# Kernel tuning notes

Hardware: AMD Instinct MI355X
Metric: run time of the kernel (lower is better)

## Reference

```python
import jax, jax.numpy as jnp
import numpy as np

B, N, F, I = 4, 1024, 32, 8
DIM, DN, NF = 256, 64, 100
H, HD = 4, 64  # heads, head_dim (H*HD == DIM)
EPS = 1e-5


def setup_inputs() -> dict:
    key = jax.random.key(0)
    ks = jax.random.split(key, 24)
    def p(k, shape, s=0.05):
        return jax.random.normal(k, shape, jnp.float32) * s
    return {
        "x": jax.random.normal(ks[0], (B, N, F, I), jnp.float32),
        "idx": jax.random.randint(ks[1], (F,), 0, NF),
        "ctx": jax.random.normal(ks[2], (B, 1, DN), jnp.float32),
        "Wp": p(ks[3], (NF, DIM * I)),          # in_projection table
        "Bp": p(ks[4], (NF, DIM)),               # feature_bias table
        "q_emb": p(ks[5], (1, DIM)),             # queries table
        "cln_kv_W": p(ks[6], (DN, 2 * DIM)), "cln_kv_b": jnp.zeros((2 * DIM,), jnp.float32),
        "cln_q_W": p(ks[7], (DN, 2 * DIM)),  "cln_q_b": jnp.zeros((2 * DIM,), jnp.float32),
        "cln_h_W": p(ks[8], (DN, 2 * DIM)),  "cln_h_b": jnp.zeros((2 * DIM,), jnp.float32),
        "Wq": p(ks[9], (DIM, DIM)), "Wk": p(ks[10], (DIM, DIM)),
        "Wv": p(ks[11], (DIM, DIM)), "Wo": p(ks[12], (DIM, DIM)),
        "W1": p(ks[13], (DIM, 4 * DIM)), "b1": jnp.zeros((4 * DIM,), jnp.float32),
        "W2": p(ks[14], (4 * DIM, DIM)), "b2": jnp.zeros((DIM,), jnp.float32),
    }


def _ln(x):
    m = x.mean(-1, keepdims=True)
    v = ((x - m) ** 2).mean(-1, keepdims=True)
    return (x - m) * jax.lax.rsqrt(v + EPS)


def _cln(x, c, W, b):
    # adaptive layernorm: ln(x) * (1 + scale(ctx)) + shift(ctx)
    h = _ln(x)
    s, sh = jnp.split(c @ W + b, 2, axis=-1)
    return h * (1.0 + s) + sh


def reference(x, idx, ctx, Wp, Bp, q_emb, cln_kv_W, cln_kv_b, cln_q_W, cln_q_b,
              cln_h_W, cln_h_b, Wq, Wk, Wv, Wo, W1, b1, W2, b2):
    b_, n_, f_, i_ = x.shape
    # gather per-feature projection weights and biases
    w = Wp[idx].reshape(f_, DIM, i_)                 # [f, d, i]
    bias = Bp[idx][None]                              # [1, f, d] (broadcasts b,n)
    kv = jnp.einsum('bnfi,fdi->bnfd', x, w)           # [b, n, f, d]
    c = ctx[:, :, None, :]                            # [b, 1, 1, dn]
    kv = _cln(kv, c, cln_kv_W, cln_kv_b) + bias
    q = jnp.broadcast_to(q_emb[None, None], (b_, n_, 1, DIM))
    # cross-attention (pre-norm, conditional)
    qn = _cln(q, c, cln_q_W, cln_q_b)
    qh = (qn @ Wq).reshape(b_, n_, 1, H, HD)
    kh = (kv @ Wk).reshape(b_, n_, f_, H, HD)
    vh = (kv @ Wv).reshape(b_, n_, f_, H, HD)
    att = jnp.einsum('bnqhe,bnfhe->bnhqf', qh, kh) / np.sqrt(HD).astype(np.float32)
    att = jax.nn.softmax(att, axis=-1)
    o = jnp.einsum('bnhqf,bnfhe->bnqhe', att, vh).reshape(b_, n_, 1, DIM) @ Wo
    h = q + o
    # MLP (pre-norm, conditional)
    hn = _cln(h, c, cln_h_W, cln_h_b)
    h = h + (jax.nn.gelu(hn @ W1 + b1) @ W2 + b2)
    return h[:, :, 0, :]                              # squeeze query dim -> [b, n, d]
```

## Files before the change

### kernel.cpp

```cpp
#include <hip/hip_runtime.h>
#include <cmath>

#define EPSV 1e-5f
using f4 = float4;

typedef __attribute__((ext_vector_type(8))) short bfrag;
typedef __attribute__((ext_vector_type(4))) float ffrag;

#define WS_SKV   0
#define WS_SHKV  1024
#define WS_SH    2048
#define WS_SHH   3072
#define WS_A     4096
#define WS_R     8192
#define WS_HT    4202496
#define WS_L     5251072
#define WS_G     6299648
#define WS_GB    WS_G
#define WS_HNB   (WS_G + 2097152)
#define WS_W1T   (WS_G + 2621440)
#define WS_W2T   (WS_G + 2752512)
#define WS_MT    (WS_G + 2883584)

#define FMA8(acc, s, wa, wb) \
  acc[0]=fmaf((s),(wa).x,acc[0]); acc[1]=fmaf((s),(wa).y,acc[1]); \
  acc[2]=fmaf((s),(wa).z,acc[2]); acc[3]=fmaf((s),(wa).w,acc[3]); \
  acc[4]=fmaf((s),(wb).x,acc[4]); acc[5]=fmaf((s),(wb).y,acc[5]); \
  acc[6]=fmaf((s),(wb).z,acc[6]); acc[7]=fmaf((s),(wb).w,acc[7]);

#define DOT8(res, v, wa, wb) \
  res = fmaf((v)[0],(wa).x,res); res = fmaf((v)[1],(wa).y,res); \
  res = fmaf((v)[2],(wa).z,res); res = fmaf((v)[3],(wa).w,res); \
  res = fmaf((v)[4],(wb).x,res); res = fmaf((v)[5],(wb).y,res); \
  res = fmaf((v)[6],(wb).z,res); res = fmaf((v)[7],(wb).w,res);

__device__ __forceinline__ float bfly32(float v){
  v += __shfl_xor(v, 1);  v += __shfl_xor(v, 2);  v += __shfl_xor(v, 4);
  v += __shfl_xor(v, 8);  v += __shfl_xor(v, 16);
  return v;
}

template<int CTRL>
__device__ __forceinline__ float dpp_add(float v){
  int x = __builtin_bit_cast(int, v);
  int y = __builtin_amdgcn_update_dpp(0, x, CTRL, 0xf, 0xf, true);
  return v + __builtin_bit_cast(float, y);
}
__device__ __forceinline__ float red32(float v){
  v = dpp_add<0xB1>(v);
  v = dpp_add<0x4E>(v);
  v = dpp_add<0x124>(v);
  v = dpp_add<0x128>(v);
  v += __shfl_xor(v, 16);
  return v;
}

__device__ __forceinline__ float gelu_fast(float x){
  float z2 = 1.5957691216057308f*(x + 0.044715f*x*x*x);
  return x / (1.0f + __expf(-z2));
}

__device__ __forceinline__ unsigned short f2bf(float x){
  union { float f; unsigned u; } v; v.f = x;
  unsigned r = v.u + 0x7fffu + ((v.u >> 16) & 1u);
  return (unsigned short)(r >> 16);
}
__device__ __forceinline__ float bfu(unsigned short u){
  union { unsigned u; float f; } v; v.u = ((unsigned)u) << 16; return v.f;
}
__device__ __forceinline__ ushort4 comb4(ushort4 a, ushort4 b, float inv){
  ushort4 r;
  r.x = f2bf((bfu(a.x)+bfu(b.x))*inv);
  r.y = f2bf((bfu(a.y)+bfu(b.y))*inv);
  r.z = f2bf((bfu(a.z)+bfu(b.z))*inv);
  r.w = f2bf((bfu(a.w)+bfu(b.w))*inv);
  return r;
}

__global__ __launch_bounds__(256) void kprep(
  const float* __restrict__ W1, const float* __restrict__ W2,
  const float* __restrict__ Wv, const float* __restrict__ Wo,
  const float* __restrict__ ctx, const float* __restrict__ q_emb,
  const float* __restrict__ Wkv, const float* __restrict__ bkv,
  const float* __restrict__ Wqc, const float* __restrict__ bqc,
  const float* __restrict__ Whc, const float* __restrict__ bhc,
  const float* __restrict__ Wq,  const float* __restrict__ Wk,
  float* __restrict__ ws)
{
  const int tid = threadIdx.x;
  int blk = blockIdx.x;
  __shared__ union {
    unsigned short lt[64][68];
    struct { float wvs[4*64]; float wos[64*256]; } m;
    struct { float c[64], qn[256], ph[256], qh64[64], red[8]; } z;
  } sm;

  if (blk < 128){
    const float* src; unsigned short* dst; int K, N, K0, N0;
    if (blk < 64){
      src = W1; dst = (unsigned short*)(ws + WS_W1T);
      K = 256; N = 1024; K0 = (blk >> 4)*64; N0 = (blk & 15)*64;
    } else {
      blk -= 64;
      src = W2; dst = (unsigned short*)(ws + WS_W2T);
      K = 1024; N = 256; K0 = (blk >> 2)*64; N0 = (blk & 3)*64;
    }
    #pragma unroll
    for (int i=0;i<4;++i){
      int r = i*16 + (tid>>4);
      int c = (tid&15)*4;
      f4 v = *(const f4*)(src + (size_t)(K0+r)*N + N0 + c);
      sm.lt[r][c]   = f2bf(v.x); sm.lt[r][c+1] = f2bf(v.y);
      sm.lt[r][c+2] = f2bf(v.z); sm.lt[r][c+3] = f2bf(v.w);
    }
    __syncthreads();
    #pragma unroll
    for (int i=0;i<4;++i){
      int n  = i*16 + (tid>>4);
      int kc = (tid&15)*4;
      ushort4 u;
      u.x = sm.lt[kc][n]; u.y = sm.lt[kc+1][n]; u.z = sm.lt[kc+2][n]; u.w = sm.lt[kc+3][n];
      *(ushort4*)(dst + (size_t)(N0+n)*K + K0 + kc) = u;
    }
  } else if (blk < 384){
    blk -= 128;
    const int h   = blk >> 6;
    const int dg4 = blk & 63;
    {
      int d = tid >> 6, e = tid & 63;
      sm.m.wvs[d*64+e] = Wv[(size_t)(dg4*4 + d)*256 + h*64 + e];
    }
    {
      int e = tid >> 2, c = (tid & 3)*64;
      const float* src = Wo + (size_t)(h*64 + e)*256 + c;
      #pragma unroll
      for (int i=0;i<16;++i)
        *(f4*)&sm.m.wos[e*256 + c + i*4] = *(const f4*)(src + i*4);
    }
    __syncthreads();
    float acc[4] = {};
    for (int e=0;e<64;++e){
      float wo = sm.m.wos[e*256 + tid];
      acc[0] = fmaf(sm.m.wvs[0*64+e], wo, acc[0]);
      acc[1] = fmaf(sm.m.wvs[1*64+e], wo, acc[1]);
      acc[2] = fmaf(sm.m.wvs[2*64+e], wo, acc[2]);
      acc[3] = fmaf(sm.m.wvs[3*64+e], wo, acc[3]);
    }
    unsigned short* Mt = (unsigned short*)(ws + WS_MT);
    ushort4 u;
    u.x = f2bf(acc[0]); u.y = f2bf(acc[1]); u.z = f2bf(acc[2]); u.w = f2bf(acc[3]);
    *(ushort4*)(Mt + (size_t)tid*1024 + h*256 + dg4*4) = u;
  } else {
    blk -= 384;
    const int b = blk >> 2, h = blk & 3;
    if (tid < 64) sm.z.c[tid] = ctx[b*64 + tid];
    __syncthreads();

    float skv = bkv[tid],      shkv = bkv[256+tid];
    float sq  = bqc[tid],      shq  = bqc[256+tid];
    float sh  = bhc[tid],      shh  = bhc[256+tid];
    #pragma unroll 8
    for (int j=0;j<64;++j){
      float cj = sm.z.c[j];
      skv  = fmaf(cj, Wkv[j*512 + tid],       skv);
      shkv = fmaf(cj, Wkv[j*512 + 256 + tid], shkv);
      sq   = fmaf(cj, Wqc[j*512 + tid],       sq);
      shq  = fmaf(cj, Wqc[j*512 + 256 + tid], shq);
      sh   = fmaf(cj, Whc[j*512 + tid],       sh);
      shh  = fmaf(cj, Whc[j*512 + 256 + tid], shh);
    }
    if (h == 0){
      ws[WS_SKV  + b*256 + tid] = skv;
      ws[WS_SHKV + b*256 + tid] = shkv;
      ws[WS_SH   + b*256 + tid] = sh;
      ws[WS_SHH  + b*256 + tid] = shh;
    }

    float qe = q_emb[tid];
    float s1r = qe, s2r = qe*qe;
    for (int mm=1;mm<64;mm<<=1){ s1r += __shfl_xor(s1r,mm); s2r += __shfl_xor(s2r,mm); }
    int wv = tid>>6, ln = tid&63;
    if (ln==0){ sm.z.red[wv*2]=s1r; sm.z.red[wv*2+1]=s2r; }
    __syncthreads();
    float S1 = sm.z.red[0]+sm.z.red[2]+sm.z.red[4]+sm.z.red[6];
    float S2 = sm.z.red[1]+sm.z.red[3]+sm.z.red[5]+sm.z.red[7];
    float mean = S1*(1.0f/256.0f);
    float var  = S2*(1.0f/256.0f) - mean*mean;
    float rs   = rsqrtf(var + EPSV);
    sm.z.qn[tid] = (qe-mean)*rs*(1.0f+sq) + shq;
    __syncthreads();

    {
      const int t = tid & 63, ks = tid >> 6;
      float p = 0.f;
      const float* wq = Wq + (size_t)(ks*64)*256 + h*64 + t;
      #pragma unroll 8
      for (int d=0; d<64; ++d) p = fmaf(sm.z.qn[ks*64+d], wq[d*256], p);
      sm.z.ph[tid] = p;
    }
    __syncthreads();
    if (tid < 64) sm.z.qh64[tid] = sm.z.ph[tid] + sm.z.ph[64+tid] + sm.z.ph[128+tid] + sm.z.ph[192+tid];
    __syncthreads();

    {
      float a = 0.f;
      const float* wkr = Wk + (size_t)tid*256 + h*64;
      #pragma unroll
      for (int e4=0; e4<16; ++e4){
        f4 wv4 = *(const f4*)(wkr + e4*4);
        a = fmaf(sm.z.qh64[e4*4+0], wv4.x, a);
        a = fmaf(sm.z.qh64[e4*4+1], wv4.y, a);
        a = fmaf(sm.z.qh64[e4*4+2], wv4.z, a);
        a = fmaf(sm.z.qh64[e4*4+3], wv4.w, a);
      }
      ws[WS_A + b*1024 + h*256 + tid] = 0.125f*a;
    }
  }
}

__global__ __launch_bounds__(256,2) void k1f_attn(
  const float* __restrict__ x, const int* __restrict__ idx,
  const float* __restrict__ Wp, const float* __restrict__ Bp,
  float* __restrict__ ws)
{
  __shared__ float xs[4096];
  __shared__ float wls[4096];

  const int tid = threadIdx.x;
  const int p0  = (blockIdx.x >> 1) * 16;
  const int half= blockIdx.x & 1;
  const int f0  = half * 16;
  const int b   = p0 >> 10;
  const int t   = tid >> 5;
  const int dg  = tid & 31;
  const int dA  = 4*dg, dB = 128 + 4*dg;

  {
    const float* xg = x + (size_t)p0*256 + tid*8;
    f4 a  = *(const f4*)xg;
    f4 bq = *(const f4*)(xg + 4);
    *(f4*)&xs[tid*8]     = a;
    *(f4*)&xs[tid*8 + 4] = bq;
    f4 a2  = *(const f4*)(xg + 2048);
    f4 bq2 = *(const f4*)(xg + 2048 + 4);
    *(f4*)&xs[2048 + tid*8]     = a2;
    *(f4*)&xs[2048 + tid*8 + 4] = bq2;
  }
  f4 Ar[4][2];
  #pragma unroll
  for (int h=0;h<4;++h){
    Ar[h][0] = *(const f4*)(ws + WS_A + b*1024 + h*256 + dA);
    Ar[h][1] = *(const f4*)(ws + WS_A + b*1024 + h*256 + dB);
  }

  f4 skA = *(const f4*)(ws + WS_SKV  + b*256 + dA);
  f4 skB = *(const f4*)(ws + WS_SKV  + b*256 + dB);
  f4 shA = *(const f4*)(ws + WS_SHKV + b*256 + dA);
  f4 shB = *(const f4*)(ws + WS_SHKV + b*256 + dB);
  float coef[8] = {1.f+skA.x,1.f+skA.y,1.f+skA.z,1.f+skA.w,
                   1.f+skB.x,1.f+skB.y,1.f+skB.z,1.f+skB.w};
  float shk[8]  = {shA.x,shA.y,shA.z,shA.w, shB.x,shB.y,shB.z,shB.w};

  int r0 = idx[f0], r1 = idx[f0+1];
  f4 u0 = *(const f4*)(Wp + (size_t)r0*2048 + tid*8);
  f4 u1 = *(const f4*)(Wp + (size_t)r0*2048 + tid*8 + 4);
  f4 u2 = *(const f4*)(Wp + (size_t)r1*2048 + tid*8);
  f4 u3 = *(const f4*)(Wp + (size_t)r1*2048 + tid*8 + 4);

  float l[2][4] = {};
  float racc[2][4][8] = {};

  for (int fi = 0; fi < 8; ++fi){
    const int f = f0 + fi*2;
    __syncthreads();
    wls[0*256+tid]=u0.x; wls[1*256+tid]=u0.y; wls[2*256+tid]=u0.z; wls[3*256+tid]=u0.w;
    wls[4*256+tid]=u1.x; wls[5*256+tid]=u1.y; wls[6*256+tid]=u1.z; wls[7*256+tid]=u1.w;
    wls[2048+0*256+tid]=u2.x; wls[2048+1*256+tid]=u2.y;
    wls[2048+2*256+tid]=u2.z; wls[2048+3*256+tid]=u2.w;
    wls[2048+4*256+tid]=u3.x; wls[2048+5*256+tid]=u3.y;
    wls[2048+6*256+tid]=u3.z; wls[2048+7*256+tid]=u3.w;
    __syncthreads();

    f4 ba0 = *(const f4*)(Bp + (size_t)r0*256 + dA);
    f4 bb0 = *(const f4*)(Bp + (size_t)r0*256 + dB);
    f4 ba1 = *(const f4*)(Bp + (size_t)r1*256 + dA);
    f4 bb1 = *(const f4*)(Bp + (size_t)r1*256 + dB);

    const int fn = (fi < 7) ? f + 2 : f0;
    int rn0 = idx[fn], rn1 = idx[fn+1];
    u0 = *(const f4*)(Wp + (size_t)rn0*2048 + tid*8);
    u1 = *(const f4*)(Wp + (size_t)rn0*2048 + tid*8 + 4);
    u2 = *(const f4*)(Wp + (size_t)rn1*2048 + tid*8);
    u3 = *(const f4*)(Wp + (size_t)rn1*2048 + tid*8 + 4);

    #pragma unroll
    for (int sub=0; sub<2; ++sub){
      const float* wrow = wls + sub*2048;
      const int fc = f + sub;
      f4 ba = sub ? ba1 : ba0;
      f4 bb = sub ? bb1 : bb0;

      float xf0[8], xf1[8];
      {
        f4 xa = *(const f4*)&xs[t*256 + fc*8];
        f4 xb = *(const f4*)&xs[t*256 + fc*8 + 4];
        xf0[0]=xa.x; xf0[1]=xa.y; xf0[2]=xa.z; xf0[3]=xa.w;
        xf0[4]=xb.x; xf0[5]=xb.y; xf0[6]=xb.z; xf0[7]=xb.w;
        f4 xc = *(const f4*)&xs[(t+8)*256 + fc*8];
        f4 xd = *(const f4*)&xs[(t+8)*256 + fc*8 + 4];
        xf1[0]=xc.x; xf1[1]=xc.y; xf1[2]=xc.z; xf1[3]=xc.w;
        xf1[4]=xd.x; xf1[5]=xd.y; xf1[6]=xd.z; xf1[7]=xd.w;
      }

      float val[2][8] = {};
      #pragma unroll
      for (int i=0;i<8;++i){
        f4 wa  = *(const f4*)&wrow[i*256 + dA];
        f4 wbv = *(const f4*)&wrow[i*256 + dB];
        FMA8(val[0], xf0[i], wa, wbv);
        FMA8(val[1], xf1[i], wa, wbv);
      }

      float off[8] = {shk[0]+ba.x, shk[1]+ba.y, shk[2]+ba.z, shk[3]+ba.w,
                      shk[4]+bb.x, shk[5]+bb.y, shk[6]+bb.z, shk[7]+bb.w};

      #pragma unroll
      for (int tt=0; tt<2; ++tt){
        float s=0.f, ss=0.f;
        #pragma unroll
        for (int jj=0;jj<8;++jj){ s += val[tt][jj]; ss = fmaf(val[tt][jj],val[tt][jj],ss); }
        s = red32(s); ss = red32(ss);
        float mean = s*(1.f/256.f);
        float var  = ss*(1.f/256.f) - mean*mean;
        float rsg  = rsqrtf(var + EPSV);
        float mrs  = mean*rsg;

        float kvl[8];
        #pragma unroll
        for (int jj=0;jj<8;++jj)
          kvl[jj] = fmaf(fmaf(val[tt][jj], rsg, -mrs), coef[jj], off[jj]);

        #pragma unroll
        for (int h=0;h<4;++h){
          float lg = 0.f;
          DOT8(lg, kvl, Ar[h][0], Ar[h][1]);
          lg = red32(lg);
          float pp = __expf(lg);
          l[tt][h] += pp;
          #pragma unroll
          for (int jj=0;jj<8;++jj)
            racc[tt][h][jj] = fmaf(pp, kvl[jj], racc[tt][h][jj]);
        }
      }
    }
    r0 = rn0; r1 = rn1;
  }

  unsigned short* Pr = (unsigned short*)(ws + WS_R);
  #pragma unroll
  for (int tt=0; tt<2; ++tt){
    size_t base = (size_t)(half*4096 + p0 + t + tt*8) * 1024;
    #pragma unroll
    for (int h=0;h<4;++h){
      ushort4 ua, ub;
      ua.x=f2bf(racc[tt][h][0]); ua.y=f2bf(racc[tt][h][1]);
      ua.z=f2bf(racc[tt][h][2]); ua.w=f2bf(racc[tt][h][3]);
      ub.x=f2bf(racc[tt][h][4]); ub.y=f2bf(racc[tt][h][5]);
      ub.z=f2bf(racc[tt][h][6]); ub.w=f2bf(racc[tt][h][7]);
      *(ushort4*)(Pr + base + h*256 + dA) = ua;
      *(ushort4*)(Pr + base + h*256 + dB) = ub;
    }
  }
  if (dg == 0){
    float* Lp = ws + WS_L;
    #pragma unroll
    for (int tt=0; tt<2; ++tt)
      #pragma unroll
      for (int h=0;h<4;++h)
        Lp[(size_t)(half*4096 + p0 + t + tt*8)*4 + h] = l[tt][h];
  }
}

__global__ __launch_bounds__(256) void k2g_mfma(float* __restrict__ ws)
{
  __shared__ unsigned short aT[2][32*40];
  __shared__ unsigned short bT[2][64*40];
  __shared__ float invs[128];
  const unsigned short* P0 = (const unsigned short*)(ws + WS_R);
  const unsigned short* P1 = P0 + 4194304;
  const unsigned short* mt = (const unsigned short*)(ws + WS_MT);
  const float* Lp = ws + WS_L;

  const int tid = threadIdx.x;
  const int M0 = (blockIdx.x >> 2) * 32;
  const int N0 = (blockIdx.x & 3) * 64;
  const int lane = tid & 63;
  const int wid = tid >> 6;
  const int wm = wid >> 1, wn = wid & 1;
  const int m16 = lane & 15, q = lane >> 4;

  const int sa_m = tid >> 3, sa_k = (tid & 7) * 4;
  const int sb_n = tid >> 2, sb_k = (tid & 3) * 8;

  if (tid < 128){
    int lt = tid >> 2, h = tid & 3;
    invs[tid] = 1.f / (Lp[(size_t)(M0 + lt)*4 + h] +
                       Lp[(size_t)(4096 + M0 + lt)*4 + h]);
  }

  ushort4 ua0 = *(const ushort4*)(P0 + (size_t)(M0 + sa_m)*1024 + sa_k);
  ushort4 ua1 = *(const ushort4*)(P1 + (size_t)(M0 + sa_m)*1024 + sa_k);
  f4 ub = *(const f4*)(mt + (size_t)(N0 + sb_n)*1024 + sb_k);
  __syncthreads();

  ffrag acc[2];
  acc[0] = (ffrag){0.f,0.f,0.f,0.f};
  acc[1] = (ffrag){0.f,0.f,0.f,0.f};

  for (int ks=0; ks<32; ++ks){
    const int buf = ks & 1;
    float inv = invs[sa_m*4 + (ks >> 3)];
    *(ushort4*)&aT[buf][sa_m*40 + sa_k] = comb4(ua0, ua1, inv);
    *(f4*)&bT[buf][sb_n*40 + sb_k]      = ub;
    __syncthreads();
    int kn = (ks < 31) ? ks+1 : 31;
    ua0 = *(const ushort4*)(P0 + (size_t)(M0 + sa_m)*1024 + kn*32 + sa_k);
    ua1 = *(const ushort4*)(P1 + (size_t)(M0 + sa_m)*1024 + kn*32 + sa_k);
    ub  = *(const f4*)(mt + (size_t)(N0 + sb_n)*1024 + kn*32 + sb_k);

    bfrag af, bf0, bf1;
    af  = *(const bfrag*)&aT[buf][(wm*16 + m16)*40 + q*8];
    bf0 = *(const bfrag*)&bT[buf][(wn*32 + m16)*40 + q*8];
    bf1 = *(const bfrag*)&bT[buf][(wn*32 + 16 + m16)*40 + q*8];
    acc[0] = __builtin_amdgcn_mfma_f32_16x16x32_bf16(bf0, af, acc[0], 0, 0, 0);
    acc[1] = __builtin_amdgcn_mfma_f32_16x16x32_bf16(bf1, af, acc[1], 0, 0, 0);
  }

  const int m = M0 + wm*16 + m16;
  #pragma unroll
  for (int j=0;j<2;++j){
    const int n4 = N0 + wn*32 + j*16 + q*4;
    *(f4*)(ws + WS_HT + (size_t)m*256 + n4) =
      make_float4(acc[j][0], acc[j][1], acc[j][2], acc[j][3]);
  }
}

__global__ __launch_bounds__(256) void ke_ln(
  const float* __restrict__ q_emb, float* __restrict__ ws)
{
  const int tid = threadIdx.x;
  const int p0 = blockIdx.x * 8;
  const int b  = p0 >> 10;
  const int tq = tid >> 5, jq = tid & 31;
  const int cA = 4*jq, cB = 128 + 4*jq;

  float* op = ws + WS_HT + (size_t)(p0+tq)*256;
  f4 oA = *(const f4*)(op + cA);
  f4 oB = *(const f4*)(op + cB);
  f4 qA = *(const f4*)(q_emb + cA);
  f4 qB = *(const f4*)(q_emb + cB);
  float ht[8] = {oA.x+qA.x, oA.y+qA.y, oA.z+qA.z, oA.w+qA.w,
                 oB.x+qB.x, oB.y+qB.y, oB.z+qB.z, oB.w+qB.w};
  float s=0.f, ss=0.f;
  #pragma unroll
  for (int jj=0;jj<8;++jj){ s += ht[jj]; ss = fmaf(ht[jj],ht[jj],ss); }
  s = bfly32(s); ss = bfly32(ss);
  float mean = s*(1.f/256.f);
  float var  = ss*(1.f/256.f) - mean*mean;
  float rsg  = rsqrtf(var + EPSV);
  f4 sH0 = *(const f4*)(ws + WS_SH  + b*256 + cA);
  f4 sH1 = *(const f4*)(ws + WS_SH  + b*256 + cB);
  f4 hH0 = *(const f4*)(ws + WS_SHH + b*256 + cA);
  f4 hH1 = *(const f4*)(ws + WS_SHH + b*256 + cB);
  float sHv[8]  = {sH0.x,sH0.y,sH0.z,sH0.w, sH1.x,sH1.y,sH1.z,sH1.w};
  float hHv[8]  = {hH0.x,hH0.y,hH0.z,hH0.w, hH1.x,hH1.y,hH1.z,hH1.w};
  float hnv[8];
  #pragma unroll
  for (int jj=0;jj<8;++jj)
    hnv[jj] = (ht[jj]-mean)*rsg*(1.f+sHv[jj]) + hHv[jj];

  *(f4*)(op+cA) = make_float4(ht[0],ht[1],ht[2],ht[3]);
  *(f4*)(op+cB) = make_float4(ht[4],ht[5],ht[6],ht[7]);
  unsigned short* hnb = (unsigned short*)(ws + WS_HNB);
  ushort4 uA, uB;
  uA.x=f2bf(hnv[0]); uA.y=f2bf(hnv[1]); uA.z=f2bf(hnv[2]); uA.w=f2bf(hnv[3]);
  uB.x=f2bf(hnv[4]); uB.y=f2bf(hnv[5]); uB.z=f2bf(hnv[6]); uB.w=f2bf(hnv[7]);
  *(ushort4*)(hnb + (size_t)(p0+tq)*256 + cA) = uA;
  *(ushort4*)(hnb + (size_t)(p0+tq)*256 + cB) = uB;
}

__global__ __launch_bounds__(256) void k3_mfma(
  const float* __restrict__ b1, float* __restrict__ ws)
{
  __shared__ unsigned short aT[2][64*40];
  __shared__ unsigned short bT[2][128*40];
  const unsigned short* hnb = (const unsigned short*)(ws + WS_HNB);
  const unsigned short* w1t = (const unsigned short*)(ws + WS_W1T);
  unsigned short* gb = (unsigned short*)(ws + WS_GB);

  const int tid = threadIdx.x;
  const int M0 = (blockIdx.x >> 3) * 64;
  const int N0 = (blockIdx.x & 7) * 128;
  const int lane = tid & 63;
  const int wid = tid >> 6;
  const int wm = wid >> 1, wn = wid & 1;
  const int m16 = lane & 15, q = lane >> 4;

  const int sa_m = tid >> 2, sa_k = (tid & 3) * 8;
  const int sb_n = tid >> 1, sb_k = (tid & 1) * 16;

  f4 ua, ub0, ub1;
  ua  = *(const f4*)(hnb + (size_t)(M0 + sa_m)*256 + sa_k);
  ub0 = *(const f4*)(w1t + (size_t)(N0 + sb_n)*256 + sb_k);
  ub1 = *(const f4*)(w1t + (size_t)(N0 + sb_n)*256 + sb_k + 8);

  ffrag acc[2][4];
  #pragma unroll
  for (int i=0;i<2;++i)
    #pragma unroll
    for (int j=0;j<4;++j) acc[i][j] = (ffrag){0.f,0.f,0.f,0.f};

  for (int ks=0; ks<8; ++ks){
    const int buf = ks & 1;
    *(f4*)&aT[buf][sa_m*40 + sa_k]     = ua;
    *(f4*)&bT[buf][sb_n*40 + sb_k]     = ub0;
    *(f4*)&bT[buf][sb_n*40 + sb_k + 8] = ub1;
    __syncthreads();
    int kn = (ks < 7) ? ks+1 : 7;
    ua  = *(const f4*)(hnb + (size_t)(M0 + sa_m)*256 + kn*32 + sa_k);
    ub0 = *(const f4*)(w1t + (size_t)(N0 + sb_n)*256 + kn*32 + sb_k);
    ub1 = *(const f4*)(w1t + (size_t)(N0 + sb_n)*256 + kn*32 + sb_k + 8);

    bfrag af[2], bf_[4];
    af[0] = *(const bfrag*)&aT[buf][(wm*32 + m16)*40 + q*8];
    af[1] = *(const bfrag*)&aT[buf][(wm*32 + 16 + m16)*40 + q*8];
    #pragma unroll
    for (int j=0;j<4;++j)
      bf_[j] = *(const bfrag*)&bT[buf][(wn*64 + j*16 + m16)*40 + q*8];
    #pragma unroll
    for (int i=0;i<2;++i)
      #pragma unroll
      for (int j=0;j<4;++j)
        acc[i][j] = __builtin_amdgcn_mfma_f32_16x16x32_bf16(bf_[j], af[i], acc[i][j], 0, 0, 0);
  }

  #pragma unroll
  for (int i=0;i<2;++i){
    const int m = M0 + wm*32 + i*16 + m16;
    #pragma unroll
    for (int j=0;j<4;++j){
      const int n4 = N0 + wn*64 + j*16 + q*4;
      f4 bv = *(const f4*)(b1 + n4);
      ushort4 u;
      u.x = f2bf(gelu_fast(acc[i][j][0] + bv.x));
      u.y = f2bf(gelu_fast(acc[i][j][1] + bv.y));
      u.z = f2bf(gelu_fast(acc[i][j][2] + bv.z));
      u.w = f2bf(gelu_fast(acc[i][j][3] + bv.w));
      *(ushort4*)(gb + (size_t)m*1024 + n4) = u;
    }
  }
}

__global__ __launch_bounds__(256) void k4_mfma(
  const float* __restrict__ b2, const float* __restrict__ ws_c,
  float* __restrict__ ws, float* __restrict__ out)
{
  __shared__ unsigned short aT[2][32*40];
  __shared__ unsigned short bT[2][64*40];
  const unsigned short* gb  = (const unsigned short*)(ws_c + WS_GB);
  const unsigned short* w2t = (const unsigned short*)(ws_c + WS_W2T);

  const int tid = threadIdx.x;
  const int M0 = (blockIdx.x >> 2) * 32;
  const int N0 = (blockIdx.x & 3) * 64;
  const int lane = tid & 63;
  const int wid = tid >> 6;
  const int wm = wid >> 1, wn = wid & 1;
  const int m16 = lane & 15, q = lane >> 4;

  const int sa_m = tid >> 3, sa_k = (tid & 7) * 4;
  const int sb_n = tid >> 2, sb_k = (tid & 3) * 8;

  ushort4 ua;
  f4 ub;
  ua = *(const ushort4*)(gb  + (size_t)(M0 + sa_m)*1024 + sa_k);
  ub = *(const f4*)(w2t + (size_t)(N0 + sb_n)*1024 + sb_k);

  ffrag acc[2];
  acc[0] = (ffrag){0.f,0.f,0.f,0.f};
  acc[1] = (ffrag){0.f,0.f,0.f,0.f};

  for (int ks=0; ks<32; ++ks){
    const int buf = ks & 1;
    *(ushort4*)&aT[buf][sa_m*40 + sa_k] = ua;
    *(f4*)&bT[buf][sb_n*40 + sb_k]      = ub;
    __syncthreads();
    int kn = (ks < 31) ? ks+1 : 31;
    ua = *(const ushort4*)(gb  + (size_t)(M0 + sa_m)*1024 + kn*32 + sa_k);
    ub = *(const f4*)(w2t + (size_t)(N0 + sb_n)*1024 + kn*32 + sb_k);

    bfrag af, bf0, bf1;
    af  = *(const bfrag*)&aT[buf][(wm*16 + m16)*40 + q*8];
    bf0 = *(const bfrag*)&bT[buf][(wn*32 + m16)*40 + q*8];
    bf1 = *(const bfrag*)&bT[buf][(wn*32 + 16 + m16)*40 + q*8];
    acc[0] = __builtin_amdgcn_mfma_f32_16x16x32_bf16(bf0, af, acc[0], 0, 0, 0);
    acc[1] = __builtin_amdgcn_mfma_f32_16x16x32_bf16(bf1, af, acc[1], 0, 0, 0);
  }

  const int m = M0 + wm*16 + m16;
  #pragma unroll
  for (int j=0;j<2;++j){
    const int n4 = N0 + wn*32 + j*16 + q*4;
    f4 bv = *(const f4*)(b2 + n4);
    f4 hv = *(const f4*)(ws + WS_HT + (size_t)m*256 + n4);
    *(f4*)(out + (size_t)m*256 + n4) =
      make_float4(acc[j][0]+bv.x+hv.x, acc[j][1]+bv.y+hv.y,
                  acc[j][2]+bv.z+hv.z, acc[j][3]+bv.w+hv.w);
  }
}

extern "C" void kernel_launch(void* const* d_in, const int* in_sizes, int n_in,
                              void* d_out, int out_size, void* d_ws, size_t ws_size,
                              hipStream_t stream)
{
  const float* x    = (const float*)d_in[0];
  const int*   idx  = (const int*)  d_in[1];
  const float* ctx  = (const float*)d_in[2];
  const float* Wp   = (const float*)d_in[3];
  const float* Bp   = (const float*)d_in[4];
  const float* qemb = (const float*)d_in[5];
  const float* Wkv  = (const float*)d_in[6];
  const float* bkv  = (const float*)d_in[7];
  const float* Wqc  = (const float*)d_in[8];
  const float* bqc  = (const float*)d_in[9];
  const float* Whc  = (const float*)d_in[10];
  const float* bhc  = (const float*)d_in[11];
  const float* Wq   = (const float*)d_in[12];
  const float* Wk   = (const float*)d_in[13];
  const float* Wv   = (const float*)d_in[14];
  const float* Wo   = (const float*)d_in[15];
  const float* W1   = (const float*)d_in[16];
  const float* b1   = (const float*)d_in[17];
  const float* W2   = (const float*)d_in[18];
  const float* b2   = (const float*)d_in[19];
  float* ws  = (float*)d_ws;
  float* out = (float*)d_out;

  hipLaunchKernelGGL(kprep,    dim3(400),  dim3(256), 0, stream,
                     W1, W2, Wv, Wo, ctx, qemb, Wkv, bkv, Wqc, bqc, Whc, bhc, Wq, Wk, ws);
  hipLaunchKernelGGL(k1f_attn, dim3(512),  dim3(256), 0, stream, x, idx, Wp, Bp, ws);
  hipLaunchKernelGGL(k2g_mfma, dim3(512),  dim3(256), 0, stream, ws);
  hipLaunchKernelGGL(ke_ln,    dim3(512),  dim3(256), 0, stream, qemb, ws);
  hipLaunchKernelGGL(k3_mfma,  dim3(512),  dim3(256), 0, stream, b1, ws);
  hipLaunchKernelGGL(k4_mfma,  dim3(512),  dim3(256), 0, stream, b2, ws, ws, out);
}
```

Baseline: 187.0 us.

## Fuse residual LayerNorm into first MLP GEMM and double-buffer weight LDS

The separate LayerNorm kernel is removed. Each block of the W1 GEMM now recomputes the conditional LayerNorm for its 64 rows and writes the bf16 result straight into LDS as the full A operand. The q_emb residual add moves into the W2 epilogue, and the k1f attention kernel double-buffers its projection-weight LDS tile so one barrier per iteration can go. This saves a launch and the round trip of the normalised activations through global memory. In exchange, the LayerNorm is recomputed eight times per row (once per N-tile block) and the GEMM kernel uses more LDS.

```diff
diff --git a/kernel.cpp b/kernel.cpp
--- a/kernel.cpp
+++ b/kernel.cpp
@@ -17,7 +17,6 @@
 #define WS_L     5251072
 #define WS_G     6299648
 #define WS_GB    WS_G
-#define WS_HNB   (WS_G + 2097152)
 #define WS_W1T   (WS_G + 2621440)
 #define WS_W2T   (WS_G + 2752512)
 #define WS_MT    (WS_G + 2883584)
@@ -224,7 +223,7 @@
   float* __restrict__ ws)
 {
   __shared__ float xs[4096];
-  __shared__ float wls[4096];
+  __shared__ float wls2[2][4096];
 
   const int tid = threadIdx.x;
   const int p0  = (blockIdx.x >> 1) * 16;
@@ -272,13 +271,13 @@
 
   for (int fi = 0; fi < 8; ++fi){
     const int f = f0 + fi*2;
-    __syncthreads();
-    wls[0*256+tid]=u0.x; wls[1*256+tid]=u0.y; wls[2*256+tid]=u0.z; wls[3*256+tid]=u0.w;
-    wls[4*256+tid]=u1.x; wls[5*256+tid]=u1.y; wls[6*256+tid]=u1.z; wls[7*256+tid]=u1.w;
-    wls[2048+0*256+tid]=u2.x; wls[2048+1*256+tid]=u2.y;
-    wls[2048+2*256+tid]=u2.z; wls[2048+3*256+tid]=u2.w;
-    wls[2048+4*256+tid]=u3.x; wls[2048+5*256+tid]=u3.y;
-    wls[2048+6*256+tid]=u3.z; wls[2048+7*256+tid]=u3.w;
+    float* wb2 = wls2[fi & 1];
+    wb2[0*256+tid]=u0.x; wb2[1*256+tid]=u0.y; wb2[2*256+tid]=u0.z; wb2[3*256+tid]=u0.w;
+    wb2[4*256+tid]=u1.x; wb2[5*256+tid]=u1.y; wb2[6*256+tid]=u1.z; wb2[7*256+tid]=u1.w;
+    wb2[2048+0*256+tid]=u2.x; wb2[2048+1*256+tid]=u2.y;
+    wb2[2048+2*256+tid]=u2.z; wb2[2048+3*256+tid]=u2.w;
+    wb2[2048+4*256+tid]=u3.x; wb2[2048+5*256+tid]=u3.y;
+    wb2[2048+6*256+tid]=u3.z; wb2[2048+7*256+tid]=u3.w;
     __syncthreads();
 
     f4 ba0 = *(const f4*)(Bp + (size_t)r0*256 + dA);
@@ -295,7 +294,7 @@
 
     #pragma unroll
     for (int sub=0; sub<2; ++sub){
-      const float* wrow = wls + sub*2048;
+      const float* wrow = wb2 + sub*2048;
       const int fc = f + sub;
       f4 ba = sub ? ba1 : ba0;
       f4 bb = sub ? bb1 : bb0;
@@ -445,72 +444,72 @@
   }
 }
 
-__global__ __launch_bounds__(256) void ke_ln(
-  const float* __restrict__ q_emb, float* __restrict__ ws)
+__global__ __launch_bounds__(256) void k3e_mfma(
+  const float* __restrict__ q_emb, const float* __restrict__ b1,
+  float* __restrict__ ws)
 {
-  const int tid = threadIdx.x;
-  const int p0 = blockIdx.x * 8;
-  const int b  = p0 >> 10;
-  const int tq = tid >> 5, jq = tid & 31;
-  const int cA = 4*jq, cB = 128 + 4*jq;
-
-  float* op = ws + WS_HT + (size_t)(p0+tq)*256;
-  f4 oA = *(const f4*)(op + cA);
-  f4 oB = *(const f4*)(op + cB);
-  f4 qA = *(const f4*)(q_emb + cA);
-  f4 qB = *(const f4*)(q_emb + cB);
-  float ht[8] = {oA.x+qA.x, oA.y+qA.y, oA.z+qA.z, oA.w+qA.w,
-                 oB.x+qB.x, oB.y+qB.y, oB.z+qB.z, oB.w+qB.w};
-  float s=0.f, ss=0.f;
-  #pragma unroll
-  for (int jj=0;jj<8;++jj){ s += ht[jj]; ss = fmaf(ht[jj],ht[jj],ss); }
-  s = bfly32(s); ss = bfly32(ss);
-  float mean = s*(1.f/256.f);
-  float var  = ss*(1.f/256.f) - mean*mean;
-  float rsg  = rsqrtf(var + EPSV);
-  f4 sH0 = *(const f4*)(ws + WS_SH  + b*256 + cA);
-  f4 sH1 = *(const f4*)(ws + WS_SH  + b*256 + cB);
-  f4 hH0 = *(const f4*)(ws + WS_SHH + b*256 + cA);
-  f4 hH1 = *(const f4*)(ws + WS_SHH + b*256 + cB);
-  float sHv[8]  = {sH0.x,sH0.y,sH0.z,sH0.w, sH1.x,sH1.y,sH1.z,sH1.w};
-  float hHv[8]  = {hH0.x,hH0.y,hH0.z,hH0.w, hH1.x,hH1.y,hH1.z,hH1.w};
-  float hnv[8];
-  #pragma unroll
-  for (int jj=0;jj<8;++jj)
-    hnv[jj] = (ht[jj]-mean)*rsg*(1.f+sHv[jj]) + hHv[jj];
-
-  *(f4*)(op+cA) = make_float4(ht[0],ht[1],ht[2],ht[3]);
-  *(f4*)(op+cB) = make_float4(ht[4],ht[5],ht[6],ht[7]);
-  unsigned short* hnb = (unsigned short*)(ws + WS_HNB);
-  ushort4 uA, uB;
-  uA.x=f2bf(hnv[0]); uA.y=f2bf(hnv[1]); uA.z=f2bf(hnv[2]); uA.w=f2bf(hnv[3]);
-  uB.x=f2bf(hnv[4]); uB.y=f2bf(hnv[5]); uB.z=f2bf(hnv[6]); uB.w=f2bf(hnv[7]);
-  *(ushort4*)(hnb + (size_t)(p0+tq)*256 + cA) = uA;
-  *(ushort4*)(hnb + (size_t)(p0+tq)*256 + cB) = uB;
-}
-
-__global__ __launch_bounds__(256) void k3_mfma(
-  const float* __restrict__ b1, float* __restrict__ ws)
-{
-  __shared__ unsigned short aT[2][64*40];
+  __shared__ unsigned short hnL[8*64*40];
   __shared__ unsigned short bT[2][128*40];
-  const unsigned short* hnb = (const unsigned short*)(ws + WS_HNB);
   const unsigned short* w1t = (const unsigned short*)(ws + WS_W1T);
   unsigned short* gb = (unsigned short*)(ws + WS_GB);
 
   const int tid = threadIdx.x;
   const int M0 = (blockIdx.x >> 3) * 64;
   const int N0 = (blockIdx.x & 7) * 128;
+  const int b  = M0 >> 10;
   const int lane = tid & 63;
   const int wid = tid >> 6;
   const int wm = wid >> 1, wn = wid & 1;
   const int m16 = lane & 15, q = lane >> 4;
 
-  const int sa_m = tid >> 2, sa_k = (tid & 3) * 8;
+  {
+    const int r  = tid >> 2;
+    const int cq = tid & 3;
+    const float* op = ws + WS_HT + (size_t)(M0 + r)*256 + cq*64;
+    const float* qp = q_emb + cq*64;
+    float s = 0.f, ssq = 0.f;
+    #pragma unroll
+    for (int i=0;i<16;++i){
+      f4 o  = *(const f4*)(op + i*4);
+      f4 qe = *(const f4*)(qp + i*4);
+      float h0 = o.x+qe.x, h1 = o.y+qe.y, h2 = o.z+qe.z, h3 = o.w+qe.w;
+      s += h0+h1+h2+h3;
+      ssq = fmaf(h0,h0,ssq); ssq = fmaf(h1,h1,ssq);
+      ssq = fmaf(h2,h2,ssq); ssq = fmaf(h3,h3,ssq);
+    }
+    s   += __shfl_xor(s, 1);   s   += __shfl_xor(s, 2);
+    ssq += __shfl_xor(ssq, 1); ssq += __shfl_xor(ssq, 2);
+    float mean = s*(1.f/256.f);
+    float var  = ssq*(1.f/256.f) - mean*mean;
+    float rsg  = rsqrtf(var + EPSV);
+    #pragma unroll
+    for (int j8=0;j8<8;++j8){
+      const int c0 = cq*64 + j8*8;
+      f4 o0 = *(const f4*)(ws + WS_HT + (size_t)(M0 + r)*256 + c0);
+      f4 o1 = *(const f4*)(ws + WS_HT + (size_t)(M0 + r)*256 + c0 + 4);
+      f4 q0 = *(const f4*)(q_emb + c0);
+      f4 q1 = *(const f4*)(q_emb + c0 + 4);
+      f4 sH0 = *(const f4*)(ws + WS_SH  + b*256 + c0);
+      f4 sH1 = *(const f4*)(ws + WS_SH  + b*256 + c0 + 4);
+      f4 hH0 = *(const f4*)(ws + WS_SHH + b*256 + c0);
+      f4 hH1 = *(const f4*)(ws + WS_SHH + b*256 + c0 + 4);
+      ushort4 u0v, u1v;
+      u0v.x = f2bf((o0.x+q0.x-mean)*rsg*(1.f+sH0.x) + hH0.x);
+      u0v.y = f2bf((o0.y+q0.y-mean)*rsg*(1.f+sH0.y) + hH0.y);
+      u0v.z = f2bf((o0.z+q0.z-mean)*rsg*(1.f+sH0.z) + hH0.z);
+      u0v.w = f2bf((o0.w+q0.w-mean)*rsg*(1.f+sH0.w) + hH0.w);
+      u1v.x = f2bf((o1.x+q1.x-mean)*rsg*(1.f+sH1.x) + hH1.x);
+      u1v.y = f2bf((o1.y+q1.y-mean)*rsg*(1.f+sH1.y) + hH1.y);
+      u1v.z = f2bf((o1.z+q1.z-mean)*rsg*(1.f+sH1.z) + hH1.z);
+      u1v.w = f2bf((o1.w+q1.w-mean)*rsg*(1.f+sH1.w) + hH1.w);
+      const int ks2 = c0 >> 5, kk = c0 & 31;
+      *(ushort4*)&hnL[ks2*2560 + r*40 + kk]     = u0v;
+      *(ushort4*)&hnL[ks2*2560 + r*40 + kk + 4] = u1v;
+    }
+  }
+
   const int sb_n = tid >> 1, sb_k = (tid & 1) * 16;
-
-  f4 ua, ub0, ub1;
-  ua  = *(const f4*)(hnb + (size_t)(M0 + sa_m)*256 + sa_k);
+  f4 ub0, ub1;
   ub0 = *(const f4*)(w1t + (size_t)(N0 + sb_n)*256 + sb_k);
   ub1 = *(const f4*)(w1t + (size_t)(N0 + sb_n)*256 + sb_k + 8);
 
@@ -522,18 +521,16 @@
 
   for (int ks=0; ks<8; ++ks){
     const int buf = ks & 1;
-    *(f4*)&aT[buf][sa_m*40 + sa_k]     = ua;
     *(f4*)&bT[buf][sb_n*40 + sb_k]     = ub0;
     *(f4*)&bT[buf][sb_n*40 + sb_k + 8] = ub1;
     __syncthreads();
     int kn = (ks < 7) ? ks+1 : 7;
-    ua  = *(const f4*)(hnb + (size_t)(M0 + sa_m)*256 + kn*32 + sa_k);
     ub0 = *(const f4*)(w1t + (size_t)(N0 + sb_n)*256 + kn*32 + sb_k);
     ub1 = *(const f4*)(w1t + (size_t)(N0 + sb_n)*256 + kn*32 + sb_k + 8);
 
     bfrag af[2], bf_[4];
-    af[0] = *(const bfrag*)&aT[buf][(wm*32 + m16)*40 + q*8];
-    af[1] = *(const bfrag*)&aT[buf][(wm*32 + 16 + m16)*40 + q*8];
+    af[0] = *(const bfrag*)&hnL[ks*2560 + (wm*32 + m16)*40 + q*8];
+    af[1] = *(const bfrag*)&hnL[ks*2560 + (wm*32 + 16 + m16)*40 + q*8];
     #pragma unroll
     for (int j=0;j<4;++j)
       bf_[j] = *(const bfrag*)&bT[buf][(wn*64 + j*16 + m16)*40 + q*8];
@@ -562,8 +559,9 @@
 }
 
 __global__ __launch_bounds__(256) void k4_mfma(
-  const float* __restrict__ b2, const float* __restrict__ ws_c,
-  float* __restrict__ ws, float* __restrict__ out)
+  const float* __restrict__ q_emb, const float* __restrict__ b2,
+  const float* __restrict__ ws_c, float* __restrict__ ws,
+  float* __restrict__ out)
 {
   __shared__ unsigned short aT[2][32*40];
   __shared__ unsigned short bT[2][64*40];
@@ -613,9 +611,10 @@
     const int n4 = N0 + wn*32 + j*16 + q*4;
     f4 bv = *(const f4*)(b2 + n4);
     f4 hv = *(const f4*)(ws + WS_HT + (size_t)m*256 + n4);
+    f4 qv = *(const f4*)(q_emb + n4);
     *(f4*)(out + (size_t)m*256 + n4) =
-      make_float4(acc[j][0]+bv.x+hv.x, acc[j][1]+bv.y+hv.y,
-                  acc[j][2]+bv.z+hv.z, acc[j][3]+bv.w+hv.w);
+      make_float4(acc[j][0]+bv.x+hv.x+qv.x, acc[j][1]+bv.y+hv.y+qv.y,
+                  acc[j][2]+bv.z+hv.z+qv.z, acc[j][3]+bv.w+hv.w+qv.w);
   }
 }
 
@@ -646,11 +645,10 @@
   float* ws  = (float*)d_ws;
   float* out = (float*)d_out;
 
-  hipLaunchKernelGGL(kprep,    dim3(400),  dim3(256), 0, stream,
+  hipLaunchKernelGGL(kprep,    dim3(400), dim3(256), 0, stream,
                      W1, W2, Wv, Wo, ctx, qemb, Wkv, bkv, Wqc, bqc, Whc, bhc, Wq, Wk, ws);
-  hipLaunchKernelGGL(k1f_attn, dim3(512),  dim3(256), 0, stream, x, idx, Wp, Bp, ws);
-  hipLaunchKernelGGL(k2g_mfma, dim3(512),  dim3(256), 0, stream, ws);
-  hipLaunchKernelGGL(ke_ln,    dim3(512),  dim3(256), 0, stream, qemb, ws);
-  hipLaunchKernelGGL(k3_mfma,  dim3(512),  dim3(256), 0, stream, b1, ws);
-  hipLaunchKernelGGL(k4_mfma,  dim3(512),  dim3(256), 0, stream, b2, ws, ws, out);
-}
+  hipLaunchKernelGGL(k1f_attn, dim3(512), dim3(256), 0, stream, x, idx, Wp, Bp, ws);
+  hipLaunchKernelGGL(k2g_mfma, dim3(512), dim3(256), 0, stream, ws);
+  hipLaunchKernelGGL(k3e_mfma, dim3(512), dim3(256), 0, stream, qemb, b1, ws);
+  hipLaunchKernelGGL(k4_mfma,  dim3(512), dim3(256), 0, stream, qemb, b2, ws, ws, out);
+}
```

Result: slower. 201.5 us (+7.7%).
